# Optimization experiments

Measured on AMD Instinct MI355X. Metric: run time of the kernel, lower is better.

The kernel has to match this reference:

```python
import jax, jax.numpy as jnp
import numpy as np

N_ATOMS = 30000
N_PAIRS = 1200000
N_BASIS = 7
N_RADIAL = 5
N_SPECIES = 119
R_MIN = 0.5
R_MAX = 6.0
UNITS = (512, 512)
BOX = 6.0  # Angstrom box edge so many pairs fall inside the cutoff
N_FEAT = 360  # gaussian-moment feature count for n_radial=5

# static triangular index sets (fully symmetric contractions)
_TRI2_I, _TRI2_J = np.triu_indices(N_RADIAL)
_TRI3 = np.array([(i, j, k) for i in range(N_RADIAL)
                  for j in range(i, N_RADIAL)
                  for k in range(j, N_RADIAL)], dtype=np.int32)


def setup_inputs() -> dict:
    key = jax.random.key(0)
    ks = jax.random.split(key, 8)
    R = jax.random.uniform(ks[0], (N_ATOMS, 3), jnp.float32) * BOX
    Z = jax.random.randint(ks[1], (N_ATOMS,), 0, N_SPECIES, dtype=jnp.int32)
    idx = jax.random.randint(ks[2], (2, N_PAIRS), 0, N_ATOMS, dtype=jnp.int32)
    W_radial = jax.random.normal(ks[3], (N_SPECIES, N_SPECIES, N_RADIAL, N_BASIS), jnp.float32) / np.sqrt(N_BASIS)
    w1 = jax.random.normal(ks[4], (N_FEAT, UNITS[0]), jnp.float32) / np.sqrt(N_FEAT)
    b1 = jnp.zeros((UNITS[0],), jnp.float32)
    w2 = jax.random.normal(ks[5], (UNITS[0], UNITS[1]), jnp.float32) / np.sqrt(UNITS[0])
    b2 = jnp.zeros((UNITS[1],), jnp.float32)
    w3 = jax.random.normal(ks[6], (UNITS[1], 1), jnp.float32) / np.sqrt(UNITS[1])
    b3 = jnp.zeros((1,), jnp.float32)
    scale = 2.0 * jnp.ones((N_SPECIES, 1), jnp.float32)
    shift = 1.0 * jnp.ones((N_SPECIES, 1), jnp.float32)
    return dict(R=R, Z=Z, idx=idx, W_radial=W_radial, w1=w1, b1=b1,
                w2=w2, b2=b2, w3=w3, b3=b3, scale=scale, shift=shift)


def _descriptor(R, Z, idx, W_radial):
    idx_i, idx_j = idx[0], idx[1]
    # pairwise displacement (free-space displacement fn)
    dr_vec = R[idx_j] - R[idx_i]                                  # [P,3]
    dr = jnp.sqrt(jnp.sum(dr_vec * dr_vec, axis=-1) + 1e-12)      # [P]
    dn = dr_vec / (dr + 1e-5)[:, None]                            # unit vectors [P,3]

    # gaussian radial basis
    betta = N_BASIS ** 2 / R_MAX ** 2
    rad_norm = (2.0 * betta / np.pi) ** 0.25
    shifts = R_MIN + (R_MAX - R_MIN) / N_BASIS * jnp.arange(N_BASIS, dtype=jnp.float32)
    basis = rad_norm * jnp.exp(-betta * (dr[:, None] - shifts) ** 2)  # [P,B]

    # cosine cutoff and per species-pair embedding of the basis
    cutoff = 0.5 * (jnp.cos(jnp.pi * dr / R_MAX) + 1.0) * (dr < R_MAX)
    coeffs = W_radial[Z[idx_i], Z[idx_j]]                          # [P,K,B] irregular gather
    radial = jnp.einsum('pkb,pb->pk', coeffs, basis)               # [P,K]
    radial = radial * (cutoff / np.sqrt(N_BASIS))[:, None]

    seg = lambda x: jax.ops.segment_sum(x, idx_i, num_segments=N_ATOMS)
    # geometric moments of order 0..3
    m0 = seg(radial)                                               # [A,K]
    m1 = seg(radial[:, :, None] * dn[:, None, :])                  # [A,K,3]
    dn2 = dn[:, :, None] * dn[:, None, :]                          # [P,3,3]
    m2 = seg(radial[:, :, None, None] * dn2[:, None])              # [A,K,3,3]
    dn3 = dn2[:, :, :, None] * dn[:, None, None, :]                # [P,3,3,3]
    m3 = seg(radial[:, :, None, None, None] * dn3[:, None])        # [A,K,3,3,3]

    # gaussian-moment invariant contractions
    c1 = jnp.einsum('ari,asi->ars', m1, m1)
    c2 = jnp.einsum('arij,asij->ars', m2, m2)
    c3 = jnp.einsum('arijk,asijk->ars', m3, m3)
    c4 = jnp.einsum('arij,asik,atjk->arst', m2, m2, m2)
    c5 = jnp.einsum('ari,asj,atij->arst', m1, m1, m2)
    c6 = jnp.einsum('arijk,asijl,atkl->arst', m3, m3, m2)
    c7 = jnp.einsum('arijk,asij,atk->arst', m3, m2, m1)

    A = m0.shape[0]
    gm = jnp.concatenate([
        m0,
        c1[:, _TRI2_I, _TRI2_J],
        c2[:, _TRI2_I, _TRI2_J],
        c3[:, _TRI2_I, _TRI2_J],
        c4[:, _TRI3[:, 0], _TRI3[:, 1], _TRI3[:, 2]],
        c5[:, _TRI2_I, _TRI2_J, :].reshape(A, -1),
        c6[:, _TRI2_I, _TRI2_J, :].reshape(A, -1),
        c7.reshape(A, -1),
    ], axis=-1)                                                    # [A,360]
    return gm


def reference(R, Z, idx, W_radial, w1, b1, w2, b2, w3, b3, scale, shift):
    gm = _descriptor(R, Z, idx, W_radial)
    h = jax.nn.swish(gm @ w1 + b1)
    h = jax.nn.swish(h @ w2 + b2)
    h = h @ w3 + b3                                                # [A,1]
    return scale[Z] * h + shift[Z]
```

## Files before the change

### kernel.cpp

```cpp
#include <hip/hip_runtime.h>

#define NA      30000
#define MPAD    30080
#define NPAIRS  1200000
#define NB      7
#define NK      5
#define NSP     119
#define NFEAT   360
#define KP1     384
#define NU      512
#define WROW    36
#define MAXSLOT 120
#define PSTRIDE 128
#define NBK     118
#define BCAP    11520
#define PPB     4688
#define NTILE   235

#define BETTA      1.3611111111111112f
#define RADNORM    0.96481348f
#define SHIFT_STEP 0.7857142857142857f
#define PI_OVER_R  0.5235987755982988f
#define INV_SQRT7  0.3779644730092272f
#define RMAXV      6.0f

typedef __attribute__((ext_vector_type(8))) short bf16x8;
typedef __attribute__((ext_vector_type(4))) float f32x4;
typedef __attribute__((ext_vector_type(2))) float f32x2;

__device__ __forceinline__ unsigned short f2b(float x) {
    unsigned u = __float_as_uint(x);
    unsigned r = u + 0x7FFF + ((u >> 16) & 1);
    return (unsigned short)(r >> 16);
}

__global__ __launch_bounds__(256)
void k_part(const int* __restrict__ idx, const int* __restrict__ Z,
            int* __restrict__ gcur, int* __restrict__ part) {
    __shared__ int hist[NBK];
    __shared__ int base[NBK];
    int tid = threadIdx.x;
    for (int b = tid; b < NBK; b += 256) hist[b] = 0;
    __syncthreads();
    int p0 = blockIdx.x * PPB;
    int p1 = min(p0 + PPB, NPAIRS);
    for (int p = p0 + tid; p < p1; p += 256)
        atomicAdd(&hist[idx[p] >> 8], 1);
    __syncthreads();
    for (int b = tid; b < NBK; b += 256) {
        base[b] = atomicAdd(&gcur[b], hist[b]);
        hist[b] = 0;
    }
    __syncthreads();
    for (int p = p0 + tid; p < p1; p += 256) {
        int i = idx[p];
        int b = i >> 8;
        int j = idx[NPAIRS + p];
        int zj = Z[j];
        int off = base[b] + atomicAdd(&hist[b], 1);
        if (off < BCAP)
            part[b * BCAP + off] = ((i & 255) << 22) | (zj << 15) | j;
    }
}

__global__ __launch_bounds__(256)
void k_csr(const int* __restrict__ part, const int* __restrict__ gcnt,
           int* __restrict__ counts, int* __restrict__ plist) {
    __shared__ int lp[128 * MAXSLOT];
    __shared__ int lc[128];
    int tid = threadIdx.x;
    int lane = tid & 63, wave = tid >> 6;
    int w = blockIdx.x;
    int cb = w >> 1;
    int par = w & 1;
    for (int t = tid; t < 128; t += 256) lc[t] = 0;
    __syncthreads();
    int n = min(gcnt[cb], BCAP);
    for (int e = tid; e < n; e += 256) {
        int v = part[cb * BCAP + e];
        int iloc = v >> 22;
        if ((iloc >> 7) == par) {
            int i7 = iloc & 127;
            int r = atomicAdd(&lc[i7], 1);
            if (r < MAXSLOT) lp[i7 * MAXSLOT + r] = v & 0x3FFFFF;
        }
    }
    __syncthreads();
    for (int t = tid; t < 128; t += 256) {
        int a = w * 128 + t;
        if (a < NA) counts[a] = min(lc[t], MAXSLOT);
    }
    for (int rr = 0; rr < 32; rr++) {
        int row = wave * 32 + rr;
        int a = w * 128 + row;
        if (a < NA) {
            for (int c = lane; c < MAXSLOT; c += 64)
                plist[(size_t)a * PSTRIDE + c] = lp[row * MAXSLOT + c];
        }
    }
}

#define PREP_W   (NSP*NSP*WROW)
#define PREP_R   NA
#define PREP_W1  (NU*KP1)
#define PREP_W2  (NU*NU)
#define PREP_TOT (PREP_W + PREP_R + PREP_W1 + PREP_W2)
__global__ void k_prep(const float* __restrict__ W, const float* __restrict__ R,
                       const float* __restrict__ w1, const float* __restrict__ w2,
                       float* __restrict__ Wp, float* __restrict__ Rp,
                       unsigned short* __restrict__ w1T, unsigned short* __restrict__ w2T) {
    int i = blockIdx.x * blockDim.x + threadIdx.x;
    if (i < PREP_W) {
        int row = i / WROW, e = i - row * WROW;
        Wp[i] = (e < NK * NB) ? W[row * (NK * NB) + e] : 0.f;
        return;
    }
    i -= PREP_W;
    if (i < PREP_R) {
        f32x4 v = {R[3*i], R[3*i+1], R[3*i+2], 0.f};
        *(f32x4*)&Rp[4*i] = v;
        return;
    }
    i -= PREP_R;
    if (i < PREP_W1) {
        int c = i / KP1, kp = i - c * KP1;
        w1T[i] = (kp < NFEAT) ? f2b(w1[kp * NU + c]) : (unsigned short)0;
        return;
    }
    i -= PREP_W1;
    if (i < PREP_W2) {
        int c = i >> 9, kp = i & 511;
        w2T[i] = f2b(w2[kp * NU + c]);
    }
}

__global__ __launch_bounds__(256, 2)
void k_moments(const float* __restrict__ Rp, const int* __restrict__ Z,
               const float* __restrict__ Wp,
               const int* __restrict__ counts,
               const int* __restrict__ plist, float* __restrict__ MT) {
    int tid = blockIdx.x * blockDim.x + threadIdx.x;
    int a = tid >> 3, q = tid & 7;
    if (a >= NA) return;
    f32x4 ri = *(const f32x4*)&Rp[4*a];
    int Zi = Z[a];
    f32x2 acc[50];
#pragma unroll
    for (int u = 0; u < 50; u++) acc[u] = (f32x2){0.f, 0.f};
    int cnt = min(counts[a], MAXSLOT);
    const int* prow = plist + (size_t)a * PSTRIDE;

    for (int t = q; t < cnt; t += 8) {
        int pk = prow[t];
        int j  = pk & 0x7FFF;
        int Zj = (pk >> 15) & 0x7F;
        f32x4 rj = *(const f32x4*)&Rp[4*j];

        const f32x4* wrow = (const f32x4*)&Wp[(Zi * NSP + Zj) * WROW];
        f32x4 w4[9];
#pragma unroll
        for (int c = 0; c < 9; c++) w4[c] = wrow[c];
        const float* wf = (const float*)w4;

        float dx = rj.x - ri.x, dy = rj.y - ri.y, dz = rj.z - ri.z;
        float d2 = dx*dx + dy*dy + dz*dz + 1e-12f;
        float dr = sqrtf(d2);
        float inv = 1.0f / (dr + 1e-5f);
        float nx = dx*inv, ny = dy*inv, nz = dz*inv;

        float basis[NB];
#pragma unroll
        for (int b = 0; b < NB; b++) {
            float tt = dr - (0.5f + SHIFT_STEP * (float)b);
            basis[b] = RADNORM * __expf(-BETTA * tt * tt);
        }
        float cut = (dr < RMAXV) ? 0.5f * (__cosf(PI_OVER_R * dr) + 1.0f) : 0.0f;
        cut *= INV_SQRT7;
        float rad[NK];
#pragma unroll
        for (int k = 0; k < NK; k++) {
            float s = 0.f;
#pragma unroll
            for (int b = 0; b < NB; b++) s += wf[k*NB + b] * basis[b];
            rad[k] = s * cut;
        }
        float g[20];
        g[0] = 1.f; g[1] = nx; g[2] = ny; g[3] = nz;
        g[4] = nx*nx; g[5] = nx*ny; g[6] = nx*nz; g[7] = ny*ny; g[8] = ny*nz; g[9] = nz*nz;
        g[10] = g[4]*nx; g[11] = g[4]*ny; g[12] = g[4]*nz; g[13] = g[5]*ny; g[14] = g[5]*nz;
        g[15] = g[6]*nz; g[16] = g[7]*ny; g[17] = g[7]*nz; g[18] = g[8]*nz; g[19] = g[9]*nz;
        f32x2 g2[10];
#pragma unroll
        for (int u = 0; u < 10; u++) g2[u] = (f32x2){g[2*u], g[2*u+1]};
#pragma unroll
        for (int k = 0; k < NK; k++) {
            f32x2 rk = (f32x2){rad[k], rad[k]};
#pragma unroll
            for (int u = 0; u < 10; u++)
                acc[k*10 + u] += rk * g2[u];
        }
    }
#pragma unroll
    for (int u = 0; u < 50; u++) {
        f32x2 v = acc[u];
        double d = __builtin_bit_cast(double, v);
        d = __shfl_xor(d, 1);
        f32x2 o = __builtin_bit_cast(f32x2, d);
        v += o;
        d = __builtin_bit_cast(double, v);
        d = __shfl_xor(d, 2);
        o = __builtin_bit_cast(f32x2, d);
        v += o;
        d = __builtin_bit_cast(double, v);
        d = __shfl_xor(d, 4);
        o = __builtin_bit_cast(f32x2, d);
        v += o;
        acc[u] = v;
    }
    if (q == 0) {
#pragma unroll
        for (int u = 0; u < 50; u++) {
            MT[(2*u)     * NA + a] = acc[u].x;
            MT[(2*u + 1) * NA + a] = acc[u].y;
        }
    }
}

__global__ __launch_bounds__(256)
void k_contract(const float* __restrict__ MT, unsigned short* __restrict__ gmB) {
    __shared__ float M[100 * 64];
    int tid = threadIdx.x;
    int lane = tid & 63;
    int wave = tid >> 6;
    int a0 = blockIdx.x * 64;
    int a = a0 + lane;

    for (int e = tid; e < 6400; e += 256) {
        int u = e >> 6, l = e & 63;
        int aa = a0 + l;
        M[e] = (aa < NA) ? MT[u * NA + aa] : 0.f;
    }
    __syncthreads();

    const int S2[3][3] = {{0,1,2},{1,3,4},{2,4,5}};
    const int S3[3][3][3] = {
        {{0,1,2},{1,3,4},{2,4,5}},
        {{1,3,4},{3,6,7},{4,7,8}},
        {{2,4,5},{4,7,8},{5,8,9}}
    };
    bool ok = (a < NA);
    unsigned short* row = gmB + (size_t)a * KP1;
#define LD(comp) M[(comp) * 64 + lane]

    if (wave == 0) {
        if (ok) {
            for (int k = 0; k < 5; k++) row[k] = f2b(LD(k * 20));
        }
        int f = 5;
        for (int r = 0; r < 5; r++)
            for (int s = r; s < 5; s++) {
                float v = 0.f;
#pragma unroll
                for (int i = 0; i < 3; i++) v += LD(r*20+1+i) * LD(s*20+1+i);
                if (ok) row[f] = f2b(v);
                f++;
            }
        const float W2U[6] = {1,2,2,1,2,1};
        for (int r = 0; r < 5; r++)
            for (int s = r; s < 5; s++) {
                float v = 0.f;
#pragma unroll
                for (int u = 0; u < 6; u++) v += W2U[u] * LD(r*20+4+u) * LD(s*20+4+u);
                if (ok) row[f] = f2b(v);
                f++;
            }
        const float W3U[10] = {1,3,3,3,6,3,1,3,3,1};
        for (int r = 0; r < 5; r++)
            for (int s = r; s < 5; s++) {
                float v = 0.f;
#pragma unroll
                for (int u = 0; u < 10; u++) v += W3U[u] * LD(r*20+10+u) * LD(s*20+10+u);
                if (ok) row[f] = f2b(v);
                f++;
            }
        for (int r = 0; r < 5; r++) {
            float m2r[6];
#pragma unroll
            for (int u = 0; u < 6; u++) m2r[u] = LD(r*20+4+u);
            for (int s = r; s < 5; s++) {
                float m2q[6];
#pragma unroll
                for (int u = 0; u < 6; u++) m2q[u] = LD(s*20+4+u);
                for (int t = s; t < 5; t++) {
                    float m2t[6];
#pragma unroll
                    for (int u = 0; u < 6; u++) m2t[u] = LD(t*20+4+u);
                    float v = 0.f;
#pragma unroll
                    for (int i = 0; i < 3; i++)
#pragma unroll
                        for (int j = 0; j < 3; j++)
#pragma unroll
                            for (int k = 0; k < 3; k++)
                                v += m2r[S2[i][j]] * m2q[S2[i][k]] * m2t[S2[j][k]];
                    if (ok) row[f] = f2b(v);
                    f++;
                }
            }
        }
    } else if (wave == 1) {
        int f = 85;
        for (int r = 0; r < 5; r++) {
            float m1r[3];
#pragma unroll
            for (int i = 0; i < 3; i++) m1r[i] = LD(r*20+1+i);
            for (int s = r; s < 5; s++) {
                float m1q[3];
#pragma unroll
                for (int i = 0; i < 3; i++) m1q[i] = LD(s*20+1+i);
                for (int t = 0; t < 5; t++) {
                    float m2t[6];
#pragma unroll
                    for (int u = 0; u < 6; u++) m2t[u] = LD(t*20+4+u);
                    float v = 0.f;
#pragma unroll
                    for (int i = 0; i < 3; i++)
#pragma unroll
                        for (int j = 0; j < 3; j++)
                            v += m1r[i] * m1q[j] * m2t[S2[i][j]];
                    if (ok) row[f] = f2b(v);
                    f++;
                }
            }
        }
        f = 235;
        for (int r = 0; r < 5; r++) {
            float m3r[10];
#pragma unroll
            for (int u = 0; u < 10; u++) m3r[u] = LD(r*20+10+u);
            for (int s = 0; s < 5; s++) {
                float m2q[6];
#pragma unroll
                for (int u = 0; u < 6; u++) m2q[u] = LD(s*20+4+u);
                float U0 = 0.f, U1 = 0.f, U2 = 0.f;
#pragma unroll
                for (int i = 0; i < 3; i++)
#pragma unroll
                    for (int j = 0; j < 3; j++) {
                        float ww = m2q[S2[i][j]];
                        U0 += m3r[S3[i][j][0]] * ww;
                        U1 += m3r[S3[i][j][1]] * ww;
                        U2 += m3r[S3[i][j][2]] * ww;
                    }
                for (int t = 0; t < 5; t++) {
                    float v = U0 * LD(t*20+1) + U1 * LD(t*20+2) + U2 * LD(t*20+3);
                    if (ok) row[f] = f2b(v);
                    f++;
                }
            }
        }
    } else {
        int pbeg = (wave == 2) ? 0 : 7;
        int pend = (wave == 2) ? 7 : 15;
        int p = 0;
        for (int r = 0; r < 5; r++)
            for (int s = r; s < 5; s++) {
                if (p >= pbeg && p < pend) {
                    float m3r[10], m3q[10];
#pragma unroll
                    for (int u = 0; u < 10; u++) m3r[u] = LD(r*20+10+u);
#pragma unroll
                    for (int u = 0; u < 10; u++) m3q[u] = LD(s*20+10+u);
                    float T[3][3];
#pragma unroll
                    for (int k = 0; k < 3; k++)
#pragma unroll
                        for (int l = 0; l < 3; l++) {
                            float v = 0.f;
#pragma unroll
                            for (int i = 0; i < 3; i++)
#pragma unroll
                                for (int j = 0; j < 3; j++)
                                    v += m3r[S3[i][j][k]] * m3q[S3[i][j][l]];
                            T[k][l] = v;
                        }
                    int f = 160 + p * 5;
                    for (int t = 0; t < 5; t++) {
                        float m2t[6];
#pragma unroll
                        for (int u = 0; u < 6; u++) m2t[u] = LD(t*20+4+u);
                        float v = 0.f;
#pragma unroll
                        for (int k = 0; k < 3; k++)
#pragma unroll
                            for (int l = 0; l < 3; l++)
                                v += T[k][l] * m2t[S2[k][l]];
                        if (ok) row[f + t] = f2b(v);
                    }
                }
                p++;
            }
        if (wave == 3 && ok) {
            for (int z = NFEAT; z < KP1; z++) row[z] = 0;
        }
    }
#undef LD
}

__device__ __forceinline__ void stage8(const unsigned short* gp, unsigned short* lp) {
    __builtin_amdgcn_global_load_lds(
        (const __attribute__((address_space(1))) unsigned int*)gp,
        (__attribute__((address_space(3))) unsigned int*)lp, 16, 0, 0);
}

template<int KPAD, int MODE>
__global__ __launch_bounds__(256) void k_mfma(const unsigned short* __restrict__ A,
                                              const unsigned short* __restrict__ B,
                                              const float* __restrict__ bias,
                                              const float* __restrict__ w3,
                                              void* __restrict__ outp) {
    __shared__ __align__(16) unsigned char SMEM[35072];
    unsigned short* As = (unsigned short*)SMEM;
    unsigned short* Bs = (unsigned short*)(SMEM + 16384);
    float* red = (float*)(SMEM + 32768);
    int tid = threadIdx.x;
    int lane = tid & 63, wave = tid >> 6;
    int wm = wave >> 1, wn = wave & 1;
    int quad = lane >> 4, l16 = lane & 15;
    int lrow = lane >> 3;
    int lchk = lane & 7;

    for (int t = 0; t < 2; t++) {
        int atile = blockIdx.y * 2 + t;
        if (atile >= NTILE) break;
        int rowA0, rowB0;
        if (MODE == 1) { rowA0 = atile * 128;      rowB0 = blockIdx.x * 128; }
        else           { rowA0 = blockIdx.x * 128; rowB0 = atile * 128; }

        f32x4 acc[4][4];
        f32x4 zero = {0.f, 0.f, 0.f, 0.f};
#pragma unroll
        for (int i = 0; i < 4; i++)
#pragma unroll
            for (int j = 0; j < 4; j++) acc[i][j] = zero;

        for (int k0 = 0; k0 < KPAD; k0 += 64) {
            __syncthreads();
#pragma unroll
            for (int i = 0; i < 4; i++) {
                int r = wave * 32 + i * 8 + lrow;
                int gc = lchk ^ (r & 7);
                stage8(A + (size_t)(rowA0 + r) * KPAD + k0 + gc * 8, &As[(wave * 32 + i * 8) * 64]);
            }
#pragma unroll
            for (int i = 0; i < 4; i++) {
                int r = wave * 32 + i * 8 + lrow;
                int gc = lchk ^ (r & 7);
                stage8(B + (size_t)(rowB0 + r) * KPAD + k0 + gc * 8, &Bs[(wave * 32 + i * 8) * 64]);
            }
            __syncthreads();
#pragma unroll
            for (int s = 0; s < 2; s++) {
                bf16x8 af[4], bfr[4];
#pragma unroll
                for (int mt = 0; mt < 4; mt++) {
                    int r = wm * 64 + mt * 16 + l16;
                    af[mt] = *(const bf16x8*)&As[r * 64 + (((s * 4 + quad) ^ (r & 7)) * 8)];
                }
#pragma unroll
                for (int nt = 0; nt < 4; nt++) {
                    int r = wn * 64 + nt * 16 + l16;
                    bfr[nt] = *(const bf16x8*)&Bs[r * 64 + (((s * 4 + quad) ^ (r & 7)) * 8)];
                }
#pragma unroll
                for (int mt = 0; mt < 4; mt++)
#pragma unroll
                    for (int nt = 0; nt < 4; nt++)
                        acc[mt][nt] = __builtin_amdgcn_mfma_f32_16x16x32_bf16(
                            af[mt], bfr[nt], acc[mt][nt], 0, 0, 0);
            }
        }

        if (MODE == 1) {
            __syncthreads();
            unsigned short* Ot = (unsigned short*)SMEM;
#pragma unroll
            for (int nt = 0; nt < 4; nt++) {
                int c_loc = wn * 64 + nt * 16 + l16;
                float b = bias[rowB0 + c_loc];
#pragma unroll
                for (int mt = 0; mt < 4; mt++) {
#pragma unroll
                    for (int reg = 0; reg < 4; reg++) {
                        int a_loc = wm * 64 + mt * 16 + quad * 4 + reg;
                        float v = acc[mt][nt][reg] + b;
                        Ot[a_loc * 136 + c_loc] = f2b(v / (1.f + __expf(-v)));
                    }
                }
            }
            __syncthreads();
            unsigned short* O = (unsigned short*)outp;
            int half = lane >> 5, l32 = lane & 31;
#pragma unroll
            for (int it = 0; it < 16; it++) {
                int rloc = wave * 32 + it * 2 + half;
                int a = rowA0 + rloc;
                unsigned long long d = *(const unsigned long long*)&Ot[rloc * 136 + l32 * 4];
                if (a < NA)
                    *(unsigned long long*)&O[(size_t)a * NU + rowB0 + l32 * 4] = d;
            }
        } else {
            float pn[4] = {0.f, 0.f, 0.f, 0.f};
#pragma unroll
            for (int mt = 0; mt < 4; mt++) {
#pragma unroll
                for (int reg = 0; reg < 4; reg++) {
                    int c = rowA0 + wm * 64 + mt * 16 + quad * 4 + reg;
                    float b = bias[c];
                    float w3c = w3[c];
#pragma unroll
                    for (int nt = 0; nt < 4; nt++) {
                        float v = acc[mt][nt][reg] + b;
                        pn[nt] += w3c * (v / (1.f + __expf(-v)));
                    }
                }
            }
#pragma unroll
            for (int nt = 0; nt < 4; nt++) {
                pn[nt] += __shfl_xor(pn[nt], 16);
                pn[nt] += __shfl_xor(pn[nt], 32);
            }
            __syncthreads();
            if (quad == 0) {
#pragma unroll
                for (int nt = 0; nt < 4; nt++)
                    red[((wm * 2 + wn) * 4 + nt) * 16 + l16] = pn[nt];
            }
            __syncthreads();
            if (tid < 128) {
                int wn2 = tid >> 6, nt2 = (tid >> 4) & 3, lb = tid & 15;
                float s = red[((0 * 2 + wn2) * 4 + nt2) * 16 + lb]
                        + red[((1 * 2 + wn2) * 4 + nt2) * 16 + lb];
                int a = rowB0 + wn2 * 64 + nt2 * 16 + lb;
                if (a < NA) atomicAdd((float*)outp + a, s);
            }
        }
    }
}

__global__ void k_finish(float* __restrict__ out, const float* __restrict__ b3,
                         const int* __restrict__ Z, const float* __restrict__ scale,
                         const float* __restrict__ shift) {
    int a = blockIdx.x * blockDim.x + threadIdx.x;
    if (a >= NA) return;
    int z = Z[a];
    out[a] = scale[z] * (out[a] + b3[0]) + shift[z];
}

extern "C" void kernel_launch(void* const* d_in, const int* in_sizes, int n_in,
                              void* d_out, int out_size, void* d_ws, size_t ws_size,
                              hipStream_t stream) {
    const float* R    = (const float*)d_in[0];
    const int*   Z    = (const int*)  d_in[1];
    const int*   idx  = (const int*)  d_in[2];
    const float* Wr   = (const float*)d_in[3];
    const float* w1   = (const float*)d_in[4];
    const float* b1   = (const float*)d_in[5];
    const float* w2   = (const float*)d_in[6];
    const float* b2   = (const float*)d_in[7];
    const float* w3   = (const float*)d_in[8];
    const float* b3   = (const float*)d_in[9];
    const float* scale= (const float*)d_in[10];
    const float* shift= (const float*)d_in[11];
    float* out = (float*)d_out;
    char* ws = (char*)d_ws;

    int*            gcur   = (int*)  (ws + 0);
    int*            counts = (int*)  (ws + 512);
    int*            part   = (int*)  (ws + 120576);
    int*            plist  = (int*)  (ws + 5558016);
    float*          MT     = (float*)(ws + 20918016);
    unsigned short* gmB    = (unsigned short*)(ws + 32918016);
    unsigned short* w1T    = (unsigned short*)(ws + 56019456);
    unsigned short* w2T    = (unsigned short*)(ws + 56412672);
    unsigned short* h1B    = (unsigned short*)(ws + 56936960);
    float*          Wpad   = (float*)(ws + 87738880);
    float*          Rpad   = (float*)(ws + 89778064);

    hipMemsetAsync(gcur, 0, 512, stream);
    hipMemsetAsync(d_out, 0, NA * sizeof(float), stream);

    k_part    <<<256, 256, 0, stream>>>(idx, Z, gcur, part);
    k_csr     <<<235, 256, 0, stream>>>(part, gcur, counts, plist);
    k_prep    <<<(PREP_TOT + 255) / 256, 256, 0, stream>>>(Wr, R, w1, w2, Wpad, Rpad, w1T, w2T);
    k_moments <<<(NA * 8 + 255) / 256, 256, 0, stream>>>(Rpad, Z, Wpad, counts, plist, MT);
    k_contract<<<(NA + 63) / 64,       256, 0, stream>>>(MT, gmB);

    k_mfma<KP1, 1><<<dim3(NU / 128, 118), 256, 0, stream>>>(gmB, w1T, b1, nullptr, (void*)h1B);
    k_mfma<NU,  2><<<dim3(NU / 128, 118), 256, 0, stream>>>(w2T, h1B, b2, w3, (void*)out);

    k_finish<<<(NA + 255) / 256, 256, 0, stream>>>(out, b3, Z, scale, shift);
}
```

Before: 268.8 us.

## Fuse moment accumulation and invariant contraction into one kernel via shared memory

```diff
diff --git a/kernel.cpp b/kernel.cpp
--- a/kernel.cpp
+++ b/kernel.cpp
@@ -108,8 +108,11 @@
 __global__ void k_prep(const float* __restrict__ W, const float* __restrict__ R,
                        const float* __restrict__ w1, const float* __restrict__ w2,
                        float* __restrict__ Wp, float* __restrict__ Rp,
-                       unsigned short* __restrict__ w1T, unsigned short* __restrict__ w2T) {
+                       unsigned short* __restrict__ w1T, unsigned short* __restrict__ w2T,
+                       int* __restrict__ gcur, float* __restrict__ out) {
     int i = blockIdx.x * blockDim.x + threadIdx.x;
+    if (i < 128) gcur[i] = 0;
+    if (i < NA) out[i] = 0.f;
     if (i < PREP_W) {
         int row = i / WROW, e = i - row * WROW;
         Wp[i] = (e < NK * NB) ? W[row * (NK * NB) + e] : 0.f;
@@ -134,123 +137,111 @@
     }
 }
 
-__global__ __launch_bounds__(256, 2)
-void k_moments(const float* __restrict__ Rp, const int* __restrict__ Z,
-               const float* __restrict__ Wp,
-               const int* __restrict__ counts,
-               const int* __restrict__ plist, float* __restrict__ MT) {
-    int tid = blockIdx.x * blockDim.x + threadIdx.x;
-    int a = tid >> 3, q = tid & 7;
-    if (a >= NA) return;
-    f32x4 ri = *(const f32x4*)&Rp[4*a];
-    int Zi = Z[a];
-    f32x2 acc[50];
-#pragma unroll
-    for (int u = 0; u < 50; u++) acc[u] = (f32x2){0.f, 0.f};
-    int cnt = min(counts[a], MAXSLOT);
-    const int* prow = plist + (size_t)a * PSTRIDE;
-
-    for (int t = q; t < cnt; t += 8) {
-        int pk = prow[t];
-        int j  = pk & 0x7FFF;
-        int Zj = (pk >> 15) & 0x7F;
-        f32x4 rj = *(const f32x4*)&Rp[4*j];
-
-        const f32x4* wrow = (const f32x4*)&Wp[(Zi * NSP + Zj) * WROW];
-        f32x4 w4[9];
-#pragma unroll
-        for (int c = 0; c < 9; c++) w4[c] = wrow[c];
-        const float* wf = (const float*)w4;
-
-        float dx = rj.x - ri.x, dy = rj.y - ri.y, dz = rj.z - ri.z;
-        float d2 = dx*dx + dy*dy + dz*dz + 1e-12f;
-        float dr = sqrtf(d2);
-        float inv = 1.0f / (dr + 1e-5f);
-        float nx = dx*inv, ny = dy*inv, nz = dz*inv;
-
-        float basis[NB];
-#pragma unroll
-        for (int b = 0; b < NB; b++) {
-            float tt = dr - (0.5f + SHIFT_STEP * (float)b);
-            basis[b] = RADNORM * __expf(-BETTA * tt * tt);
-        }
-        float cut = (dr < RMAXV) ? 0.5f * (__cosf(PI_OVER_R * dr) + 1.0f) : 0.0f;
-        cut *= INV_SQRT7;
-        float rad[NK];
-#pragma unroll
-        for (int k = 0; k < NK; k++) {
-            float s = 0.f;
-#pragma unroll
-            for (int b = 0; b < NB; b++) s += wf[k*NB + b] * basis[b];
-            rad[k] = s * cut;
-        }
-        float g[20];
-        g[0] = 1.f; g[1] = nx; g[2] = ny; g[3] = nz;
-        g[4] = nx*nx; g[5] = nx*ny; g[6] = nx*nz; g[7] = ny*ny; g[8] = ny*nz; g[9] = nz*nz;
-        g[10] = g[4]*nx; g[11] = g[4]*ny; g[12] = g[4]*nz; g[13] = g[5]*ny; g[14] = g[5]*nz;
-        g[15] = g[6]*nz; g[16] = g[7]*ny; g[17] = g[7]*nz; g[18] = g[8]*nz; g[19] = g[9]*nz;
-        f32x2 g2[10];
-#pragma unroll
-        for (int u = 0; u < 10; u++) g2[u] = (f32x2){g[2*u], g[2*u+1]};
-#pragma unroll
-        for (int k = 0; k < NK; k++) {
-            f32x2 rk = (f32x2){rad[k], rad[k]};
-#pragma unroll
-            for (int u = 0; u < 10; u++)
-                acc[k*10 + u] += rk * g2[u];
-        }
-    }
-#pragma unroll
-    for (int u = 0; u < 50; u++) {
-        f32x2 v = acc[u];
-        double d = __builtin_bit_cast(double, v);
-        d = __shfl_xor(d, 1);
-        f32x2 o = __builtin_bit_cast(f32x2, d);
-        v += o;
-        d = __builtin_bit_cast(double, v);
-        d = __shfl_xor(d, 2);
-        o = __builtin_bit_cast(f32x2, d);
-        v += o;
-        d = __builtin_bit_cast(double, v);
-        d = __shfl_xor(d, 4);
-        o = __builtin_bit_cast(f32x2, d);
-        v += o;
-        acc[u] = v;
-    }
-    if (q == 0) {
+__global__ __launch_bounds__(512, 2)
+void k_momcon(const float* __restrict__ Rp, const int* __restrict__ Z,
+              const float* __restrict__ Wp, const int* __restrict__ counts,
+              const int* __restrict__ plist, unsigned short* __restrict__ gmB) {
+    __shared__ float MS[100 * 65];
+    int tid = threadIdx.x;
+    int g = tid >> 3, q = tid & 7;
+    int a0 = blockIdx.x * 64;
+    int a = a0 + g;
+
+    if (a < NA) {
+        f32x4 ri = *(const f32x4*)&Rp[4*a];
+        int Zi = Z[a];
+        f32x2 acc[50];
+#pragma unroll
+        for (int u = 0; u < 50; u++) acc[u] = (f32x2){0.f, 0.f};
+        int cnt = min(counts[a], MAXSLOT);
+        const int* prow = plist + (size_t)a * PSTRIDE;
+
+        for (int t = q; t < cnt; t += 8) {
+            int pk = prow[t];
+            int j  = pk & 0x7FFF;
+            int Zj = (pk >> 15) & 0x7F;
+            f32x4 rj = *(const f32x4*)&Rp[4*j];
+
+            const f32x4* wrow = (const f32x4*)&Wp[(Zi * NSP + Zj) * WROW];
+            f32x4 w4[9];
+#pragma unroll
+            for (int c = 0; c < 9; c++) w4[c] = wrow[c];
+            const float* wf = (const float*)w4;
+
+            float dx = rj.x - ri.x, dy = rj.y - ri.y, dz = rj.z - ri.z;
+            float d2 = dx*dx + dy*dy + dz*dz + 1e-12f;
+            float dr = sqrtf(d2);
+            float inv = 1.0f / (dr + 1e-5f);
+            float nx = dx*inv, ny = dy*inv, nz = dz*inv;
+
+            float basis[NB];
+#pragma unroll
+            for (int b = 0; b < NB; b++) {
+                float tt = dr - (0.5f + SHIFT_STEP * (float)b);
+                basis[b] = RADNORM * __expf(-BETTA * tt * tt);
+            }
+            float cut = (dr < RMAXV) ? 0.5f * (__cosf(PI_OVER_R * dr) + 1.0f) : 0.0f;
+            cut *= INV_SQRT7;
+            float rad[NK];
+#pragma unroll
+            for (int k = 0; k < NK; k++) {
+                float s = 0.f;
+#pragma unroll
+                for (int b = 0; b < NB; b++) s += wf[k*NB + b] * basis[b];
+                rad[k] = s * cut;
+            }
+            float gg[20];
+            gg[0] = 1.f; gg[1] = nx; gg[2] = ny; gg[3] = nz;
+            gg[4] = nx*nx; gg[5] = nx*ny; gg[6] = nx*nz; gg[7] = ny*ny; gg[8] = ny*nz; gg[9] = nz*nz;
+            gg[10] = gg[4]*nx; gg[11] = gg[4]*ny; gg[12] = gg[4]*nz; gg[13] = gg[5]*ny; gg[14] = gg[5]*nz;
+            gg[15] = gg[6]*nz; gg[16] = gg[7]*ny; gg[17] = gg[7]*nz; gg[18] = gg[8]*nz; gg[19] = gg[9]*nz;
+            f32x2 g2[10];
+#pragma unroll
+            for (int u = 0; u < 10; u++) g2[u] = (f32x2){gg[2*u], gg[2*u+1]};
+#pragma unroll
+            for (int k = 0; k < NK; k++) {
+                f32x2 rk = (f32x2){rad[k], rad[k]};
+#pragma unroll
+                for (int u = 0; u < 10; u++)
+                    acc[k*10 + u] += rk * g2[u];
+            }
+        }
 #pragma unroll
         for (int u = 0; u < 50; u++) {
-            MT[(2*u)     * NA + a] = acc[u].x;
-            MT[(2*u + 1) * NA + a] = acc[u].y;
-        }
-    }
-}
-
-__global__ __launch_bounds__(256)
-void k_contract(const float* __restrict__ MT, unsigned short* __restrict__ gmB) {
-    __shared__ float M[100 * 64];
-    int tid = threadIdx.x;
-    int lane = tid & 63;
-    int wave = tid >> 6;
-    int a0 = blockIdx.x * 64;
-    int a = a0 + lane;
-
-    for (int e = tid; e < 6400; e += 256) {
-        int u = e >> 6, l = e & 63;
-        int aa = a0 + l;
-        M[e] = (aa < NA) ? MT[u * NA + aa] : 0.f;
+            f32x2 v = acc[u];
+            double d = __builtin_bit_cast(double, v);
+            d = __shfl_xor(d, 1);
+            v += __builtin_bit_cast(f32x2, d);
+            d = __builtin_bit_cast(double, v);
+            d = __shfl_xor(d, 2);
+            v += __builtin_bit_cast(f32x2, d);
+            d = __builtin_bit_cast(double, v);
+            d = __shfl_xor(d, 4);
+            v += __builtin_bit_cast(f32x2, d);
+            acc[u] = v;
+        }
+        if (q == 0) {
+#pragma unroll
+            for (int u = 0; u < 50; u++) {
+                MS[(2*u)     * 65 + g] = acc[u].x;
+                MS[(2*u + 1) * 65 + g] = acc[u].y;
+            }
+        }
     }
     __syncthreads();
 
+    int lane = tid & 63, wave = tid >> 6;
+    if (wave >= 4) return;
+    int aB = a0 + lane;
+    bool ok = (aB < NA);
     const int S2[3][3] = {{0,1,2},{1,3,4},{2,4,5}};
     const int S3[3][3][3] = {
         {{0,1,2},{1,3,4},{2,4,5}},
         {{1,3,4},{3,6,7},{4,7,8}},
         {{2,4,5},{4,7,8},{5,8,9}}
     };
-    bool ok = (a < NA);
-    unsigned short* row = gmB + (size_t)a * KP1;
-#define LD(comp) M[(comp) * 64 + lane]
+    unsigned short* row = gmB + (size_t)aB * KP1;
+#define LD(comp) MS[(comp) * 65 + lane]
 
     if (wave == 0) {
         if (ok) {
@@ -579,7 +570,6 @@
     int*            counts = (int*)  (ws + 512);
     int*            part   = (int*)  (ws + 120576);
     int*            plist  = (int*)  (ws + 5558016);
-    float*          MT     = (float*)(ws + 20918016);
     unsigned short* gmB    = (unsigned short*)(ws + 32918016);
     unsigned short* w1T    = (unsigned short*)(ws + 56019456);
     unsigned short* w2T    = (unsigned short*)(ws + 56412672);
@@ -587,14 +577,11 @@
     float*          Wpad   = (float*)(ws + 87738880);
     float*          Rpad   = (float*)(ws + 89778064);
 
-    hipMemsetAsync(gcur, 0, 512, stream);
-    hipMemsetAsync(d_out, 0, NA * sizeof(float), stream);
-
-    k_part    <<<256, 256, 0, stream>>>(idx, Z, gcur, part);
-    k_csr     <<<235, 256, 0, stream>>>(part, gcur, counts, plist);
-    k_prep    <<<(PREP_TOT + 255) / 256, 256, 0, stream>>>(Wr, R, w1, w2, Wpad, Rpad, w1T, w2T);
-    k_moments <<<(NA * 8 + 255) / 256, 256, 0, stream>>>(Rpad, Z, Wpad, counts, plist, MT);
-    k_contract<<<(NA + 63) / 64,       256, 0, stream>>>(MT, gmB);
+    k_prep   <<<(PREP_TOT + 255) / 256, 256, 0, stream>>>(Wr, R, w1, w2, Wpad, Rpad,
+                                                          w1T, w2T, gcur, out);
+    k_part   <<<256, 256, 0, stream>>>(idx, Z, gcur, part);
+    k_csr    <<<235, 256, 0, stream>>>(part, gcur, counts, plist);
+    k_momcon <<<(NA + 63) / 64, 512, 0, stream>>>(Rpad, Z, Wpad, counts, plist, gmB);
 
     k_mfma<KP1, 1><<<dim3(NU / 128, 118), 256, 0, stream>>>(gmB, w1T, b1, nullptr, (void*)h1B);
     k_mfma<NU,  2><<<dim3(NU / 128, 118), 256, 0, stream>>>(w2T, h1B, b2, w3, (void*)out);
```

Result: faster. 258.6 us (-3.8%).
